# Kernel tuning notes

Hardware: AMD Instinct MI355X
Metric: run time of the kernel (lower is better)

## Reference

```python
import jax, jax.numpy as jnp
import numpy as np

N_NODES = 50000
N_EDGES = 600000
N_COMM = 500
COMM_EDGES = 8000
NFEAT = 128
NHID = 128
NCLASS = 10
NLAYERS = 3
NHEADS = 8
EPS = 1e-5


def setup_inputs() -> dict:
    key = jax.random.key(0)
    ks = jax.random.split(key, 32)
    s = 0.05
    def rn(i, shape, scale=s):
        return (jax.random.normal(ks[i], shape, dtype=jnp.float32) * scale)
    return {
        "node_features": jax.random.normal(ks[0], (N_NODES, NFEAT), dtype=jnp.float32),
        "node_edge_index": jax.random.randint(ks[1], (2, N_EDGES), 0, N_NODES),
        "comm_features": jax.random.normal(ks[2], (N_COMM, NHID), dtype=jnp.float32),
        "comm_edge_index": jax.random.randint(ks[3], (2, COMM_EDGES), 0, N_COMM),
        "node_to_comm_map": jax.random.randint(ks[4], (N_NODES,), 0, N_COMM),
        # node-branch GCN params (nfeat == nhid so weights stack)
        "node_W": rn(5, (NLAYERS, NHID, NHID)),
        "node_b": rn(6, (NLAYERS, NHID)),
        "node_bn_g": 1.0 + rn(7, (NLAYERS, NHID)),
        "node_bn_b": rn(8, (NLAYERS, NHID)),
        # community-branch GCN params
        "comm_W": rn(9, (NLAYERS, NHID, NHID)),
        "comm_b": rn(10, (NLAYERS, NHID)),
        "comm_bn_g": 1.0 + rn(11, (NLAYERS, NHID)),
        "comm_bn_b": rn(12, (NLAYERS, NHID)),
        # MultiheadAttention params (torch layout: y = x @ W.T + b)
        "attn_in_w": rn(13, (3 * NHID, NHID)),
        "attn_in_b": rn(14, (3 * NHID,)),
        "attn_out_w": rn(15, (NHID, NHID)),
        "attn_out_b": rn(16, (NHID,)),
        # gate LayerNorm
        "ln_g": 1.0 + rn(17, (NHID,)),
        "ln_b": rn(18, (NHID,)),
        # classifier: Linear(128,64) -> BN -> ReLU -> Linear(64,10)
        "cls_W1": rn(19, (NHID, NHID // 2)),
        "cls_b1": rn(20, (NHID // 2,)),
        "cls_bn_g": 1.0 + rn(21, (NHID // 2,)),
        "cls_bn_b": rn(22, (NHID // 2,)),
        "cls_W2": rn(23, (NHID // 2, NCLASS)),
        "cls_b2": rn(24, (NCLASS,)),
    }


def _gcn_norm(edge_index, n):
    # PyG gcn_norm: add self-loops, symmetric D^-1/2 (A+I) D^-1/2
    loop = jnp.arange(n)
    src = jnp.concatenate([edge_index[0], loop])
    dst = jnp.concatenate([edge_index[1], loop])
    deg = jax.ops.segment_sum(jnp.ones(src.shape[0], jnp.float32), dst, num_segments=n)
    dinv = jnp.where(deg > 0, deg ** -0.5, 0.0)
    return src, dst, dinv[src] * dinv[dst]


def _gcn_stack(x, edge_index, Ws, bs, gs, betas):
    n = x.shape[0]
    src, dst, norm = _gcn_norm(edge_index, n)
    h = x
    for i in range(Ws.shape[0]):
        h_prev = h
        m = h @ Ws[i]  # linear commutes with normalized aggregation
        agg = jax.ops.segment_sum(m[src] * norm[:, None], dst, num_segments=n) + bs[i]
        mu = agg.mean(0)
        var = agg.var(0)  # biased, as torch BN training
        hb = (agg - mu) / jnp.sqrt(var + EPS) * gs[i] + betas[i]
        h = jax.nn.relu(hb)
        if i > 0:
            h = h + h_prev
    return h


def _mha(x, wi, bi, wo, bo):
    # x: [N, S=2, E]
    N, S, E = x.shape
    dh = E // NHEADS
    qkv = x @ wi.T + bi
    q, k, v = jnp.split(qkv, 3, axis=-1)
    q = q.reshape(N, S, NHEADS, dh)
    k = k.reshape(N, S, NHEADS, dh)
    v = v.reshape(N, S, NHEADS, dh)
    att = jnp.einsum('nqhd,nkhd->nhqk', q, k) / np.float32(np.sqrt(dh))
    att = jax.nn.softmax(att, axis=-1)
    o = jnp.einsum('nhqk,nkhd->nqhd', att, v).reshape(N, S, E)
    return o @ wo.T + bo


def reference(node_features, node_edge_index, comm_features, comm_edge_index,
              node_to_comm_map, node_W, node_b, node_bn_g, node_bn_b,
              comm_W, comm_b, comm_bn_g, comm_bn_b,
              attn_in_w, attn_in_b, attn_out_w, attn_out_b,
              ln_g, ln_b, cls_W1, cls_b1, cls_bn_g, cls_bn_b, cls_W2, cls_b2):
    h_node = _gcn_stack(node_features, node_edge_index, node_W, node_b, node_bn_g, node_bn_b)
    h_comm = _gcn_stack(comm_features, comm_edge_index, comm_W, comm_b, comm_bn_g, comm_bn_b)
    safe = jnp.clip(node_to_comm_map, 0, h_comm.shape[0] - 1)
    h_comm_exp = h_comm[safe]  # [N, nhid] cross-scale gather
    comb = jnp.stack([h_node, h_comm_exp], axis=1)  # [N, 2, nhid]
    attended = _mha(comb, attn_in_w, attn_in_b, attn_out_w, attn_out_b)
    x = attended.mean(axis=1) + h_node
    mu = x.mean(-1, keepdims=True)
    var = x.var(-1, keepdims=True)
    h_final = (x - mu) / jnp.sqrt(var + EPS) * ln_g + ln_b
    z = h_final @ cls_W1 + cls_b1
    zm = z.mean(0)
    zv = z.var(0)
    z = jax.nn.relu((z - zm) / jnp.sqrt(zv + EPS) * cls_bn_g + cls_bn_b)
    logits = z @ cls_W2 + cls_b2
    return jax.nn.log_softmax(logits, axis=-1)
```

## Files before the change

kernel.cpp:

```cpp
#include <hip/hip_runtime.h>
#include <hip/hip_bf16.h>
#include <cstdint>
#include <cstddef>


typedef __attribute__((ext_vector_type(8))) short bf16x8;
typedef __attribute__((ext_vector_type(4))) float f32x4;

#define EPSV 1e-5f

__device__ __forceinline__ float b2f(unsigned short u) {
    union { unsigned int i; float f; } x; x.i = ((unsigned int)u) << 16; return x.f;
}
__device__ __forceinline__ unsigned short f2b(float f) {
    union { float f; unsigned int i; } x; x.f = f;
    unsigned int i = x.i;
    return (unsigned short)((i + 0x7fffu + ((i >> 16) & 1u)) >> 16);
}

__global__ void prep_kernel(const float* __restrict__ node_W, const float* __restrict__ comm_W,
                            const float* __restrict__ cls_W1, const float* __restrict__ attn_in_w,
                            const float* __restrict__ attn_out_w, const float* __restrict__ comm_feat,
                            const float* __restrict__ node_feat,
                            unsigned short* __restrict__ WtN, unsigned short* __restrict__ WtC,
                            unsigned short* __restrict__ W1t, unsigned short* __restrict__ WinB,
                            unsigned short* __restrict__ WoutB, unsigned short* __restrict__ cfb,
                            unsigned short* __restrict__ nfb, int nC128, int nN128) {
    int idx = blockIdx.x * 256 + threadIdx.x;
    if (idx < 49152) {
        int l = idx >> 14, e = idx & 16383;
        int j = e & 7, lane = (e >> 3) & 63, kc = (e >> 9) & 3, t = e >> 11;
        int col = t * 16 + (lane & 15);
        int k = (lane >> 4) * 8 + kc * 32 + j;
        WtN[idx] = f2b(node_W[l * 16384 + k * 128 + col]); return;
    }
    idx -= 49152;
    if (idx < 49152) {
        int l = idx >> 14, e = idx & 16383;
        int j = e & 7, lane = (e >> 3) & 63, kc = (e >> 9) & 3, t = e >> 11;
        int col = t * 16 + (lane & 15);
        int k = (lane >> 4) * 8 + kc * 32 + j;
        WtC[idx] = f2b(comm_W[l * 16384 + k * 128 + col]); return;
    }
    idx -= 49152;
    if (idx < 8192) {
        int e = idx;
        int j = e & 7, lane = (e >> 3) & 63, kc = (e >> 9) & 3, t = e >> 11;
        int col = t * 16 + (lane & 15);
        int k = (lane >> 4) * 8 + kc * 32 + j;
        W1t[idx] = f2b(cls_W1[k * 64 + col]); return;
    }
    idx -= 8192;
    if (idx < 49152) {
        int e = idx;
        int j = e & 7, lane = (e >> 3) & 63, kc = (e >> 9) & 3, t = e >> 11;
        int col = t * 16 + (lane & 15);
        int k = (lane >> 4) * 8 + kc * 32 + j;
        WinB[idx] = f2b(attn_in_w[col * 128 + k]); return;
    }
    idx -= 49152;
    if (idx < 16384) {
        int e = idx;
        int j = e & 7, lane = (e >> 3) & 63, kc = (e >> 9) & 3, t = e >> 11;
        int col = t * 16 + (lane & 15);
        int k = (lane >> 4) * 8 + kc * 32 + j;
        WoutB[idx] = f2b(attn_out_w[col * 128 + k]); return;
    }
    idx -= 16384;
    if (idx < nC128) { cfb[idx] = f2b(comm_feat[idx]); return; }
    idx -= nC128;
    if (idx < nN128) { nfb[idx] = f2b(node_feat[idx]); }
}

__global__ void count_dual(const int* __restrict__ nd, int* __restrict__ cnt_n, int nE,
                           const int* __restrict__ cd, int* __restrict__ cnt_c, int cE) {
    int t = blockIdx.x * 256 + threadIdx.x;
    if (t < nE) atomicAdd(&cnt_n[nd[t]], 1);
    else if (t - nE < cE) atomicAdd(&cnt_c[cd[t - nE]], 1);
}

__global__ void scan_block_dual(const int* __restrict__ cnt_n, int* __restrict__ rs_n,
                                int* __restrict__ bsum_n, int nN, int nbN,
                                const int* __restrict__ cnt_c, int* __restrict__ rs_c,
                                int* __restrict__ bsum_c, int nC,
                                float* __restrict__ di_n, float* __restrict__ di_c) {
    __shared__ int tmp[2048];
    int extra = (int)blockIdx.x - (nbN + (int)((nC + 1023) >> 10));
    int nbC = (nC + 1023) >> 10;
    extra = (int)blockIdx.x - (nbN + nbC);
    if (extra >= 0) {
        int g = extra * 1024 + (int)threadIdx.x;
        if (g < nN) di_n[g] = rsqrtf((float)cnt_n[g] + 1.0f);
        else { int gc = g - nN; if (gc < nC) di_c[gc] = rsqrtf((float)cnt_c[gc] + 1.0f); }
        return;
    }
    const int* cnt; int* excl; int* bsum; int n, lb;
    if ((int)blockIdx.x < nbN) { cnt = cnt_n; excl = rs_n; bsum = bsum_n; n = nN; lb = blockIdx.x; }
    else { cnt = cnt_c; excl = rs_c; bsum = bsum_c; n = nC; lb = blockIdx.x - nbN; }
    int tid = threadIdx.x;
    int gid = lb * 1024 + tid;
    int v = (gid < n) ? ((cnt[gid] + 7) & ~7) : 0;
    int buf = 0;
    tmp[tid] = v;
    __syncthreads();
    for (int d = 1; d < 1024; d <<= 1) {
        int t = tmp[buf * 1024 + tid];
        int add = (tid >= d) ? tmp[buf * 1024 + tid - d] : 0;
        tmp[(1 - buf) * 1024 + tid] = t + add;
        buf = 1 - buf;
        __syncthreads();
    }
    int inc = tmp[buf * 1024 + tid];
    if (gid < n) excl[gid] = inc - v;
    if (tid == 1023) bsum[lb] = inc;
}

__global__ void scan_sums_dual(int* __restrict__ bsum_n, int nbN,
                               int* __restrict__ bsum_c, int nbC) {
    if (threadIdx.x == 0) {
        int acc = 0;
        for (int i = 0; i < nbN; ++i) { int t = bsum_n[i]; bsum_n[i] = acc; acc += t; }
    } else if (threadIdx.x == 1) {
        int acc = 0;
        for (int i = 0; i < nbC; ++i) { int t = bsum_c[i]; bsum_c[i] = acc; acc += t; }
    }
}

__global__ void scan_add_dual(int* __restrict__ rs_n, const int* __restrict__ bsum_n,
                              int* __restrict__ cur_n, int nN,
                              int* __restrict__ rs_c, const int* __restrict__ bsum_c,
                              int* __restrict__ cur_c, int nC) {
    int gid = blockIdx.x * 256 + threadIdx.x;
    if (gid < nN) {
        int v = rs_n[gid] + bsum_n[gid >> 10];
        rs_n[gid] = v; cur_n[gid] = v;
    } else {
        int g = gid - nN;
        if (g < nC) {
            int v = rs_c[g] + bsum_c[g >> 10];
            rs_c[g] = v; cur_c[g] = v;
        }
    }
}

__global__ void fill_dual(const int* __restrict__ ns, const int* __restrict__ ndst,
                          int* __restrict__ cur_n, int* __restrict__ csrc_n, int nE,
                          const int* __restrict__ cs, const int* __restrict__ cdst,
                          int* __restrict__ cur_c, int* __restrict__ csrc_c, int cE) {
    int e = blockIdx.x * 256 + threadIdx.x;
    if (e < nE) {
        int s = ns[e], d = ndst[e];
        int pos = atomicAdd(&cur_n[d], 1);
        __builtin_nontemporal_store(s, csrc_n + pos);
    } else if (e - nE < cE) {
        int ee = e - nE;
        int s = cs[ee], d = cdst[ee];
        int pos = atomicAdd(&cur_c[d], 1);
        __builtin_nontemporal_store(s, csrc_c + pos);
    }
}

__device__ __forceinline__ void gemm_wave_128(const unsigned short* __restrict__ A,
                                              const unsigned short* __restrict__ Bt,
                                              const float* __restrict__ di,
                                              unsigned short* __restrict__ D,
                                              int M, int m0, int lane) {
    int r = lane & 15, q = lane >> 4;
    int arow = m0 + r; if (arow >= M) arow = M - 1;
    const unsigned short* ap = A + (size_t)arow * 128 + q * 8;
    bf16x8 afrag[4];
#pragma unroll
    for (int kc = 0; kc < 4; ++kc)
        afrag[kc] = *(const bf16x8*)(const void*)(ap + kc * 32);
    float dsc[4];
#pragma unroll
    for (int t = 0; t < 4; ++t) {
        int row = m0 + q * 4 + t; if (row >= M) row = M - 1;
        dsc[t] = di[row];
    }
#pragma unroll
    for (int tt = 0; tt < 8; ++tt) {
        f32x4 acc = {0.f, 0.f, 0.f, 0.f};
#pragma unroll
        for (int kc = 0; kc < 4; ++kc) {
            bf16x8 bfrag = *(const bf16x8*)(const void*)(Bt + (((size_t)tt * 4 + kc) << 9) + lane * 8);
            acc = __builtin_amdgcn_mfma_f32_16x16x32_bf16(afrag[kc], bfrag, acc, 0, 0, 0);
        }
        int n0 = tt * 16;
#pragma unroll
        for (int t = 0; t < 4; ++t) {
            int row = m0 + q * 4 + t;
            if (row < M) D[(size_t)row * 128 + n0 + r] = f2b(acc[t] * dsc[t]);
        }
    }
}

__global__ __launch_bounds__(256) void gemm_dual(
    const unsigned short* __restrict__ A0, const unsigned short* __restrict__ Bt0,
    const float* __restrict__ di0, unsigned short* __restrict__ D0, int M0, int blocksA,
    const unsigned short* __restrict__ A1, const unsigned short* __restrict__ Bt1,
    const float* __restrict__ di1, unsigned short* __restrict__ D1, int M1) {
    int blk = blockIdx.x;
    const unsigned short *A, *Bt; const float* di; unsigned short* D; int M, lb;
    if (blk < blocksA) { A = A0; Bt = Bt0; di = di0; D = D0; M = M0; lb = blk; }
    else { A = A1; Bt = Bt1; di = di1; D = D1; M = M1; lb = blk - blocksA; }
    int m0 = (lb * 4 + (int)(threadIdx.x >> 6)) * 16;
    if (m0 >= M) return;
    gemm_wave_128(A, Bt, di, D, M, m0, threadIdx.x & 63);
}

__global__ void gemm_kernel(const unsigned short* __restrict__ A,
                            const unsigned short* __restrict__ Bt,
                            const float* __restrict__ bias,
                            float* __restrict__ D, int M, int Ncol) {
    int wave = (blockIdx.x * blockDim.x + threadIdx.x) >> 6;
    int lane = threadIdx.x & 63;
    int m0 = wave * 16;
    if (m0 >= M) return;
    int r = lane & 15, q = lane >> 4;
    int arow = m0 + r; if (arow >= M) arow = M - 1;
    const unsigned short* ap = A + (size_t)arow * 128 + q * 8;
    bf16x8 afrag[4];
#pragma unroll
    for (int kc = 0; kc < 4; ++kc)
        afrag[kc] = *(const bf16x8*)(const void*)(ap + kc * 32);
    int ntiles = Ncol >> 4;
    for (int tt = 0; tt < ntiles; ++tt) {
        f32x4 acc = {0.f, 0.f, 0.f, 0.f};
#pragma unroll
        for (int kc = 0; kc < 4; ++kc) {
            bf16x8 bfrag = *(const bf16x8*)(const void*)(Bt + (((size_t)tt * 4 + kc) << 9) + lane * 8);
            acc = __builtin_amdgcn_mfma_f32_16x16x32_bf16(afrag[kc], bfrag, acc, 0, 0, 0);
        }
        int n0 = tt * 16;
        float bv = bias[n0 + r];
#pragma unroll
        for (int t = 0; t < 4; ++t) {
            int row = m0 + q * 4 + t;
            if (row < M) D[(size_t)row * Ncol + n0 + r] = acc[t] + bv;
        }
    }
}

__global__ __launch_bounds__(256) void gather_dual(
    const unsigned short* __restrict__ m0, const int* __restrict__ rs0,
    const int* __restrict__ cnt0, const int* __restrict__ cs0,
    const float* __restrict__ di0, const float* __restrict__ b0,
    float* __restrict__ agg0, float* __restrict__ bins0, int n0, int blocksA,
    const unsigned short* __restrict__ m1, const int* __restrict__ rs1,
    const int* __restrict__ cnt1, const int* __restrict__ cs1,
    const float* __restrict__ di1, const float* __restrict__ b1,
    float* __restrict__ agg1, float* __restrict__ bins1, int n1) {
    __shared__ float lsum[4][128], lsq[4][128];
    int blk = blockIdx.x;
    const unsigned short* m; const int *rs, *cnt, *cs; const float *di, *bias;
    float *agg, *bins; int n, lb;
    if (blk < blocksA) { m = m0; rs = rs0; cnt = cnt0; cs = cs0; di = di0; bias = b0; agg = agg0; bins = bins0; n = n0; lb = blk; }
    else { m = m1; rs = rs1; cnt = cnt1; cs = cs1; di = di1; bias = b1; agg = agg1; bins = bins1; n = n1; lb = blk - blocksA; }
    int wib = threadIdx.x >> 6, lane = threadIdx.x & 63;
    int node = lb * 4 + wib;
    bool act = node < n;
    float a0 = 0.f, a1 = 0.f;
    if (act) {
        int start = rs[node];
        int end = start + ((cnt[node] + 7) & ~7);
        for (int i = start; i < end; i += 8) {
            int s[8]; unsigned int v[8];
#pragma unroll
            for (int j = 0; j < 8; ++j) s[j] = cs[i + j];
#pragma unroll
            for (int j = 0; j < 8; ++j) {
                int si = s[j] < 0 ? node : s[j];
                v[j] = *(const unsigned int*)(m + (size_t)si * 128 + 2 * lane);
            }
#pragma unroll
            for (int j = 0; j < 8; ++j) {
                float wj = s[j] >= 0 ? 1.f : 0.f;
                a0 += b2f((unsigned short)(v[j] & 0xffff)) * wj;
                a1 += b2f((unsigned short)(v[j] >> 16)) * wj;
            }
        }
        unsigned int v = *(const unsigned int*)(m + (size_t)node * 128 + 2 * lane);
        a0 += b2f((unsigned short)(v & 0xffff));
        a1 += b2f((unsigned short)(v >> 16));
        float d = di[node];
        a0 = a0 * d + bias[2 * lane];
        a1 = a1 * d + bias[2 * lane + 1];
        float2 o; o.x = a0; o.y = a1;
        ((float2*)(agg + (size_t)node * 128))[lane] = o;
    }
    lsum[wib][2 * lane] = a0;       lsum[wib][2 * lane + 1] = a1;
    lsq[wib][2 * lane] = a0 * a0;   lsq[wib][2 * lane + 1] = a1 * a1;
    __syncthreads();
    int t = threadIdx.x;
    int bb = (lb & 31) * 256;
    if (t < 128) {
        float v = lsum[0][t] + lsum[1][t] + lsum[2][t] + lsum[3][t];
        atomicAdd(&bins[bb + t], v);
    } else {
        int c = t - 128;
        float v = lsq[0][c] + lsq[1][c] + lsq[2][c] + lsq[3][c];
        atomicAdd(&bins[bb + 128 + c], v);
    }
}

__global__ void stats_fin_dual(float* __restrict__ bins0, float* __restrict__ s0,
                               float* __restrict__ bins1, float* __restrict__ s1) {
    int t = threadIdx.x;
    float a = 0.f;
#pragma unroll
    for (int b = 0; b < 32; ++b) { a += bins0[b * 256 + t]; bins0[b * 256 + t] = 0.f; }
    s0[t] = a;
    float c = 0.f;
#pragma unroll
    for (int b = 0; b < 32; ++b) { c += bins1[b * 256 + t]; bins1[b * 256 + t] = 0.f; }
    s1[t] = c;
}

__global__ __launch_bounds__(256) void apply_dual(
    const float* __restrict__ agg0, const float* __restrict__ sums0,
    const float* __restrict__ g0, const float* __restrict__ be0,
    unsigned short* __restrict__ hb0, int n0, int blocksA, int useRes,
    const float* __restrict__ agg1, const float* __restrict__ sums1,
    const float* __restrict__ g1, const float* __restrict__ be1,
    unsigned short* __restrict__ hb1, int n1) {
    __shared__ float sc[128], sh[128];
    int blk = blockIdx.x;
    const float *agg, *sums, *g, *be; unsigned short* hb; int n, lb;
    if (blk < blocksA) { agg = agg0; sums = sums0; g = g0; be = be0; hb = hb0; n = n0; lb = blk; }
    else { agg = agg1; sums = sums1; g = g1; be = be1; hb = hb1; n = n1; lb = blk - blocksA; }
    int t = threadIdx.x;
    if (t < 128) {
        float inv = 1.f / (float)n;
        float mean = sums[t] * inv;
        float var = sums[128 + t] * inv - mean * mean;
        float rstd = rsqrtf(var + EPSV);
        float s = g[t] * rstd;
        sc[t] = s;
        sh[t] = be[t] - mean * s;
    }
    __syncthreads();
    int base = lb * 1024 + t * 4;
    if (base < n * 128) {
        float4 a = *(const float4*)(agg + base);
        ushort4 h = *(const ushort4*)(hb + base);
        int f = base & 127;
        float v0 = fmaxf(a.x * sc[f] + sh[f], 0.f);
        float v1 = fmaxf(a.y * sc[f + 1] + sh[f + 1], 0.f);
        float v2 = fmaxf(a.z * sc[f + 2] + sh[f + 2], 0.f);
        float v3 = fmaxf(a.w * sc[f + 3] + sh[f + 3], 0.f);
        if (useRes) { v0 += b2f(h.x); v1 += b2f(h.y); v2 += b2f(h.z); v3 += b2f(h.w); }
        ushort4 o; o.x = f2b(v0); o.y = f2b(v1); o.z = f2b(v2); o.w = f2b(v3);
        *(ushort4*)(hb + base) = o;
    }
}

__global__ __launch_bounds__(256) void mha_fused_kernel(
    const unsigned short* __restrict__ hbn, const int* __restrict__ map,
    const float* __restrict__ cqkv,
    const unsigned short* __restrict__ WinB, const float* __restrict__ bin,
    const unsigned short* __restrict__ WoutB, const float* __restrict__ bout,
    const float* __restrict__ lng, const float* __restrict__ lnb,
    unsigned short* __restrict__ hfin, int nN, int nC) {
    __shared__ unsigned short obf_s[16 * 144];
    __shared__ float att_s[16 * 132];

    int b = blockIdx.x;
    int hg = threadIdx.x >> 6;
    int lane = threadIdx.x & 63;
    int r = lane & 15, q = lane >> 4;

    int arow = b * 16 + r; if (arow >= nN) arow = nN - 1;
    const unsigned short* ap = hbn + (size_t)arow * 128 + q * 8;
    bf16x8 afrag[4];
#pragma unroll
    for (int kc = 0; kc < 4; ++kc)
        afrag[kc] = *(const bf16x8*)(const void*)(ap + kc * 32);

    const float* cp[4];
#pragma unroll
    for (int t = 0; t < 4; ++t) {
        int nt = b * 16 + q * 4 + t; if (nt >= nN) nt = nN - 1;
        int c = map[nt]; c = c < 0 ? 0 : (c >= nC ? nC - 1 : c);
        cp[t] = cqkv + (size_t)c * 384;
    }

#pragma unroll
    for (int c = 0; c < 2; ++c) {
        int h = hg * 2 + c;
        f32x4 qa, ka, va;
#pragma unroll
        for (int p = 0; p < 3; ++p) {
            int tt = p * 8 + h;
            f32x4 acc = {0.f, 0.f, 0.f, 0.f};
#pragma unroll
            for (int kc = 0; kc < 4; ++kc) {
                bf16x8 bfrag = *(const bf16x8*)(const void*)(WinB + (((size_t)tt * 4 + kc) << 9) + lane * 8);
                acc = __builtin_amdgcn_mfma_f32_16x16x32_bf16(afrag[kc], bfrag, acc, 0, 0, 0);
            }
            float bv = bin[tt * 16 + r];
#pragma unroll
            for (int t = 0; t < 4; ++t) acc[t] += bv;
            if (p == 0) qa = acc; else if (p == 1) ka = acc; else va = acc;
        }
        float qc[4], kc_[4], vc[4];
#pragma unroll
        for (int t = 0; t < 4; ++t) {
            const float* cpt = cp[t] + h * 16 + r;
            qc[t] = cpt[0]; kc_[t] = cpt[128]; vc[t] = cpt[256];
        }
#pragma unroll
        for (int t = 0; t < 4; ++t) {
            float s00 = qa[t] * ka[t];
            float s01 = qa[t] * kc_[t];
            float s10 = qc[t] * ka[t];
            float s11 = qc[t] * kc_[t];
#pragma unroll
            for (int mku = 1; mku <= 8; mku <<= 1) {
                s00 += __shfl_xor(s00, mku); s01 += __shfl_xor(s01, mku);
                s10 += __shfl_xor(s10, mku); s11 += __shfl_xor(s11, mku);
            }
            s00 *= 0.25f; s01 *= 0.25f; s10 *= 0.25f; s11 *= 0.25f;
            float m0 = fmaxf(s00, s01), m1 = fmaxf(s10, s11);
            float e00 = __expf(s00 - m0), e01 = __expf(s01 - m0);
            float e10 = __expf(s10 - m1), e11 = __expf(s11 - m1);
            float i0 = 1.f / (e00 + e01), i1 = 1.f / (e10 + e11);
            float o0 = (e00 * va[t] + e01 * vc[t]) * i0;
            float o1 = (e10 * va[t] + e11 * vc[t]) * i1;
            obf_s[(q * 4 + t) * 144 + h * 16 + r] = f2b(0.5f * (o0 + o1));
        }
    }
    __syncthreads();

    bf16x8 ofrag[4];
#pragma unroll
    for (int kc = 0; kc < 4; ++kc)
        ofrag[kc] = *(const bf16x8*)(const void*)(obf_s + r * 144 + q * 8 + kc * 32);
#pragma unroll
    for (int c = 0; c < 2; ++c) {
        int tt = hg * 2 + c;
        f32x4 acc = {0.f, 0.f, 0.f, 0.f};
#pragma unroll
        for (int kc = 0; kc < 4; ++kc) {
            bf16x8 bfrag = *(const bf16x8*)(const void*)(WoutB + (((size_t)tt * 4 + kc) << 9) + lane * 8);
            acc = __builtin_amdgcn_mfma_f32_16x16x32_bf16(ofrag[kc], bfrag, acc, 0, 0, 0);
        }
        int n0 = tt * 16;
        float bv = bout[n0 + r];
#pragma unroll
        for (int t = 0; t < 4; ++t)
            att_s[(q * 4 + t) * 132 + n0 + r] = acc[t] + bv;
    }
    __syncthreads();

    {
        int nl = threadIdx.x >> 4;
        int j = threadIdx.x & 15;
        int gnode = b * 16 + nl;
        bool ok = gnode < nN; if (!ok) gnode = nN - 1;
        const unsigned short* hrow = hbn + (size_t)gnode * 128 + j * 8;
        ushort4 ha = *(const ushort4*)(hrow);
        ushort4 hbv = *(const ushort4*)(hrow + 4);
        float x[8]; float s = 0.f, s2 = 0.f;
        x[0] = att_s[nl * 132 + j * 8 + 0] + b2f(ha.x);
        x[1] = att_s[nl * 132 + j * 8 + 1] + b2f(ha.y);
        x[2] = att_s[nl * 132 + j * 8 + 2] + b2f(ha.z);
        x[3] = att_s[nl * 132 + j * 8 + 3] + b2f(ha.w);
        x[4] = att_s[nl * 132 + j * 8 + 4] + b2f(hbv.x);
        x[5] = att_s[nl * 132 + j * 8 + 5] + b2f(hbv.y);
        x[6] = att_s[nl * 132 + j * 8 + 6] + b2f(hbv.z);
        x[7] = att_s[nl * 132 + j * 8 + 7] + b2f(hbv.w);
#pragma unroll
        for (int i = 0; i < 8; ++i) { s += x[i]; s2 += x[i] * x[i]; }
        s += __shfl_xor(s, 1);  s2 += __shfl_xor(s2, 1);
        s += __shfl_xor(s, 2);  s2 += __shfl_xor(s2, 2);
        s += __shfl_xor(s, 4);  s2 += __shfl_xor(s2, 4);
        s += __shfl_xor(s, 8);  s2 += __shfl_xor(s2, 8);
        float mu = s * (1.f / 128.f);
        float var = s2 * (1.f / 128.f) - mu * mu;
        float rstd = rsqrtf(var + EPSV);
        if (ok) {
            ushort4 o1, o2;
            o1.x = f2b((x[0] - mu) * rstd * lng[j * 8 + 0] + lnb[j * 8 + 0]);
            o1.y = f2b((x[1] - mu) * rstd * lng[j * 8 + 1] + lnb[j * 8 + 1]);
            o1.z = f2b((x[2] - mu) * rstd * lng[j * 8 + 2] + lnb[j * 8 + 2]);
            o1.w = f2b((x[3] - mu) * rstd * lng[j * 8 + 3] + lnb[j * 8 + 3]);
            o2.x = f2b((x[4] - mu) * rstd * lng[j * 8 + 4] + lnb[j * 8 + 4]);
            o2.y = f2b((x[5] - mu) * rstd * lng[j * 8 + 5] + lnb[j * 8 + 5]);
            o2.z = f2b((x[6] - mu) * rstd * lng[j * 8 + 6] + lnb[j * 8 + 6]);
            o2.w = f2b((x[7] - mu) * rstd * lng[j * 8 + 7] + lnb[j * 8 + 7]);
            *(ushort4*)(hfin + (size_t)gnode * 128 + j * 8) = o1;
            *(ushort4*)(hfin + (size_t)gnode * 128 + j * 8 + 4) = o2;
        }
    }
}

__global__ __launch_bounds__(256) void stats64_kernel(const float* __restrict__ z,
                                                      float* __restrict__ sums, int N) {
    __shared__ float ls[4][64], lsq[4][64];
    int f = threadIdx.x & 63, rg = threadIdx.x >> 6;
    int r0 = blockIdx.x * 64 + rg * 16;
    int r1 = r0 + 16; if (r1 > N) r1 = N;
    float s = 0.f, s2 = 0.f;
    for (int r = r0; r < r1; ++r) {
        float v = z[(size_t)r * 64 + f];
        s += v; s2 += v * v;
    }
    ls[rg][f] = s; lsq[rg][f] = s2;
    __syncthreads();
    int t = threadIdx.x;
    if (t < 64) atomicAdd(&sums[t], ls[0][t] + ls[1][t] + ls[2][t] + ls[3][t]);
    else if (t < 128) { int c = t - 64; atomicAdd(&sums[64 + c], lsq[0][c] + lsq[1][c] + lsq[2][c] + lsq[3][c]); }
}

__global__ __launch_bounds__(256) void final_kernel(const float* __restrict__ z,
                                                    const float* __restrict__ sums,
                                                    const float* __restrict__ g,
                                                    const float* __restrict__ be,
                                                    const float* __restrict__ W2,
                                                    const float* __restrict__ b2v,
                                                    float* __restrict__ out, int nN) {
    int node = blockIdx.x * 4 + (threadIdx.x >> 6);
    int lane = threadIdx.x & 63;
    float inv = 1.f / (float)nN;
    float mean = sums[lane] * inv;
    float var = sums[64 + lane] * inv - mean * mean;
    float sc = g[lane] * rsqrtf(var + EPSV);
    float sh = be[lane] - mean * sc;
    float v = 0.f;
    if (node < nN) v = fmaxf(z[(size_t)node * 64 + lane] * sc + sh, 0.f);
    float p[10];
    const float* wrow = W2 + lane * 10;
#pragma unroll
    for (int c = 0; c < 10; ++c) p[c] = v * wrow[c];
#pragma unroll
    for (int off = 32; off >= 1; off >>= 1) {
#pragma unroll
        for (int c = 0; c < 10; ++c) p[c] += __shfl_xor(p[c], off);
    }
    if (node >= nN) return;
    float l[10], mx = -1e30f;
#pragma unroll
    for (int c = 0; c < 10; ++c) { l[c] = p[c] + b2v[c]; mx = fmaxf(mx, l[c]); }
    float se = 0.f;
#pragma unroll
    for (int c = 0; c < 10; ++c) se += expf(l[c] - mx);
    float lse = mx + logf(se);
    if (lane < 10) out[(size_t)node * 10 + lane] = l[lane] - lse;
}

static inline int cdiv(long a, long b) { return (int)((a + b - 1) / b); }

extern "C" void kernel_launch(void* const* d_in, const int* in_sizes, int n_in,
                              void* d_out, int out_size, void* d_ws, size_t ws_size,
                              hipStream_t stream) {
    const float* node_feat = (const float*)d_in[0];
    const int*   nedge     = (const int*)d_in[1];
    const float* comm_feat = (const float*)d_in[2];
    const int*   cedge     = (const int*)d_in[3];
    const int*   n2c       = (const int*)d_in[4];
    const float* node_W    = (const float*)d_in[5];
    const float* node_b    = (const float*)d_in[6];
    const float* node_g    = (const float*)d_in[7];
    const float* node_beta = (const float*)d_in[8];
    const float* comm_W    = (const float*)d_in[9];
    const float* comm_b    = (const float*)d_in[10];
    const float* comm_g    = (const float*)d_in[11];
    const float* comm_beta = (const float*)d_in[12];
    const float* attn_in_w = (const float*)d_in[13];
    const float* attn_in_b = (const float*)d_in[14];
    const float* attn_out_w= (const float*)d_in[15];
    const float* attn_out_b= (const float*)d_in[16];
    const float* ln_g      = (const float*)d_in[17];
    const float* ln_b      = (const float*)d_in[18];
    const float* cls_W1    = (const float*)d_in[19];
    const float* cls_b1    = (const float*)d_in[20];
    const float* cls_bn_g  = (const float*)d_in[21];
    const float* cls_bn_b  = (const float*)d_in[22];
    const float* cls_W2    = (const float*)d_in[23];
    const float* cls_b2    = (const float*)d_in[24];

    const int nN = in_sizes[0] / 128;
    const int nE = in_sizes[1] / 2;
    const int nC = in_sizes[2] / 128;
    const int cE = in_sizes[3] / 2;
    const int padE_n = nE + 8 * nN;
    const int padE_c = cE + 8 * nC;

    char* ws = (char*)d_ws;
    size_t off = 0;
    auto alloc = [&](size_t bytes) -> char* {
        char* p = ws + off;
        off = (off + bytes + 255) & ~(size_t)255;
        return p;
    };
    size_t zero_begin = off;
    int*   cnt_n  = (int*)alloc((size_t)nN * 4);
    int*   cur_n  = (int*)alloc((size_t)nN * 4);
    int*   cnt_c  = (int*)alloc((size_t)nC * 4);
    int*   cur_c  = (int*)alloc((size_t)nC * 4);
    float* gsums  = (float*)alloc((size_t)6 * 256 * 4);
    float* csums  = (float*)alloc(128 * 4);
    float* bins_n = (float*)alloc((size_t)32 * 256 * 4);
    float* bins_c = (float*)alloc((size_t)32 * 256 * 4);
    size_t zero_bytes = off - zero_begin;
    size_t neg_begin = off;
    int*   csrc_n = (int*)alloc((size_t)padE_n * 4);
    int*   csrc_c = (int*)alloc((size_t)padE_c * 4);
    size_t neg_bytes = off - neg_begin;
    int*   rs_n   = (int*)alloc((size_t)(nN + 1) * 4);
    int*   bsum_n = (int*)alloc(256 * 4);
    float* dinv_n = (float*)alloc((size_t)nN * 4);
    int*   rs_c   = (int*)alloc((size_t)(nC + 1) * 4);
    int*   bsum_c = (int*)alloc(256 * 4);
    float* dinv_c = (float*)alloc((size_t)nC * 4);
    unsigned short* hb_n  = (unsigned short*)alloc((size_t)nN * 256);
    unsigned short* hb_c  = (unsigned short*)alloc((size_t)nC * 256);
    unsigned short* cfb   = (unsigned short*)alloc((size_t)nC * 256);
    unsigned short* m_cb  = (unsigned short*)alloc((size_t)nC * 256);
    float*          agg_c = (float*)alloc((size_t)nC * 512);
    float*          cqkv  = (float*)alloc((size_t)nC * 384 * 4);
    unsigned short* WtN  = (unsigned short*)alloc((size_t)3 * 16384 * 2);
    unsigned short* WtC  = (unsigned short*)alloc((size_t)3 * 16384 * 2);
    unsigned short* W1t  = (unsigned short*)alloc((size_t)64 * 128 * 2);
    unsigned short* WinB = (unsigned short*)alloc((size_t)384 * 128 * 2);
    unsigned short* WoutB= (unsigned short*)alloc((size_t)128 * 128 * 2);
    unsigned short* m_nb = (unsigned short*)alloc((size_t)nN * 256);
    float*          agg_n= (float*)alloc((size_t)nN * 512);
    unsigned short* nfb  = (unsigned short*)agg_n;
    unsigned short* hfin = m_nb;
    float*          z    = agg_n;

    hipMemsetAsync(ws + zero_begin, 0, zero_bytes, stream);
    hipMemsetAsync(ws + neg_begin, 0xFF, neg_bytes, stream);

    long prepN = 49152L * 3 + 8192 + 16384 + (long)nC * 128 + (long)nN * 128;
    prep_kernel<<<cdiv(prepN, 256), 256, 0, stream>>>(
        node_W, comm_W, cls_W1, attn_in_w, attn_out_w, comm_feat, node_feat,
        WtN, WtC, W1t, WinB, WoutB, cfb, nfb, nC * 128, nN * 128);

    count_dual<<<cdiv((long)nE + cE, 256), 256, 0, stream>>>(nedge + nE, cnt_n, nE, cedge + cE, cnt_c, cE);
    int nbN = cdiv(nN, 1024), nbC = cdiv(nC, 1024);
    int dinvB = cdiv((long)nN + nC, 1024);
    scan_block_dual<<<nbN + nbC + dinvB, 1024, 0, stream>>>(
        cnt_n, rs_n, bsum_n, nN, nbN, cnt_c, rs_c, bsum_c, nC, dinv_n, dinv_c);
    scan_sums_dual<<<1, 64, 0, stream>>>(bsum_n, nbN, bsum_c, nbC);
    scan_add_dual<<<cdiv((long)nN + nC, 256), 256, 0, stream>>>(
        rs_n, bsum_n, cur_n, nN, rs_c, bsum_c, cur_c, nC);
    fill_dual<<<cdiv((long)nE + cE, 256), 256, 0, stream>>>(
        nedge, nedge + nE, cur_n, csrc_n, nE,
        cedge, cedge + cE, cur_c, csrc_c, cE);

    int gemmA = cdiv(nN, 64), gemmB = cdiv(nC, 64);
    int gatA = cdiv(nN, 4), gatB = cdiv(nC, 4);
    int appA = cdiv((long)nN * 128, 1024), appB = cdiv((long)nC * 128, 1024);
    for (int i = 0; i < 3; ++i) {
        const unsigned short* A0 = i == 0 ? nfb : hb_n;
        const unsigned short* A1 = i == 0 ? cfb : hb_c;
        float* s0 = gsums + (size_t)(i * 2 + 0) * 256;
        float* s1 = gsums + (size_t)(i * 2 + 1) * 256;
        gemm_dual<<<gemmA + gemmB, 256, 0, stream>>>(
            A0, WtN + i * 16384, dinv_n, m_nb, nN, gemmA,
            A1, WtC + i * 16384, dinv_c, m_cb, nC);
        gather_dual<<<gatA + gatB, 256, 0, stream>>>(
            m_nb, rs_n, cnt_n, csrc_n, dinv_n, node_b + i * 128, agg_n, bins_n, nN, gatA,
            m_cb, rs_c, cnt_c, csrc_c, dinv_c, comm_b + i * 128, agg_c, bins_c, nC);
        stats_fin_dual<<<1, 256, 0, stream>>>(bins_n, s0, bins_c, s1);
        apply_dual<<<appA + appB, 256, 0, stream>>>(
            agg_n, s0, node_g + i * 128, node_beta + i * 128, hb_n, nN, appA, i > 0 ? 1 : 0,
            agg_c, s1, comm_g + i * 128, comm_beta + i * 128, hb_c, nC);
    }

    int cwaves = cdiv(nC, 16);
    gemm_kernel<<<cdiv((long)cwaves * 64, 256), 256, 0, stream>>>(
        hb_c, WinB, attn_in_b, cqkv, nC, 384);

    mha_fused_kernel<<<cdiv(nN, 16), 256, 0, stream>>>(
        hb_n, n2c, cqkv, WinB, attn_in_b, WoutB, attn_out_b, ln_g, ln_b, hfin, nN, nC);

    int waves1 = (nN + 15) / 16;
    gemm_kernel<<<cdiv((long)waves1 * 64, 256), 256, 0, stream>>>(
        hfin, W1t, cls_b1, z, nN, 64);
    stats64_kernel<<<cdiv(nN, 64), 256, 0, stream>>>(z, csums, nN);
    final_kernel<<<cdiv(nN, 4), 256, 0, stream>>>(z, csums, cls_bn_g, cls_bn_b,
                                                  cls_W2, cls_b2, (float*)d_out, nN);
}
```

Measured before the change: 508.3 us.

## Give each wave its own 16-node tile in fused MHA and drop block barriers

The fused attention kernel now assigns one 16-node tile per wave, with four tiles per block, instead of splitting 8 heads across 4 waves of a single tile. Each wave computes all heads, its own output projection and the LayerNorm in registers using shuffles. This removes the two block-wide syncs and the float staging buffer in shared memory. In exchange each wave does four times more MFMA work per tile and reloads all weight fragments. The residual reads and output writes become scalar 2-byte accesses rather than vectorized ones.

```diff
diff --git a/kernel.cpp b/kernel.cpp
--- a/kernel.cpp
+++ b/kernel.cpp
@@ -85,9 +85,8 @@
                                 int* __restrict__ bsum_c, int nC,
                                 float* __restrict__ di_n, float* __restrict__ di_c) {
     __shared__ int tmp[2048];
-    int extra = (int)blockIdx.x - (nbN + (int)((nC + 1023) >> 10));
     int nbC = (nC + 1023) >> 10;
-    extra = (int)blockIdx.x - (nbN + nbC);
+    int extra = (int)blockIdx.x - (nbN + nbC);
     if (extra >= 0) {
         int g = extra * 1024 + (int)threadIdx.x;
         if (g < nN) di_n[g] = rsqrtf((float)cnt_n[g] + 1.0f);
@@ -362,15 +361,14 @@
     const unsigned short* __restrict__ WoutB, const float* __restrict__ bout,
     const float* __restrict__ lng, const float* __restrict__ lnb,
     unsigned short* __restrict__ hfin, int nN, int nC) {
-    __shared__ unsigned short obf_s[16 * 144];
-    __shared__ float att_s[16 * 132];
-
-    int b = blockIdx.x;
-    int hg = threadIdx.x >> 6;
+    __shared__ unsigned short obf_s[4][16 * 136];
+
+    int w = threadIdx.x >> 6;
     int lane = threadIdx.x & 63;
     int r = lane & 15, q = lane >> 4;
-
-    int arow = b * 16 + r; if (arow >= nN) arow = nN - 1;
+    int gbase = blockIdx.x * 64 + w * 16;
+
+    int arow = gbase + r; if (arow >= nN) arow = nN - 1;
     const unsigned short* ap = hbn + (size_t)arow * 128 + q * 8;
     bf16x8 afrag[4];
 #pragma unroll
@@ -380,14 +378,15 @@
     const float* cp[4];
 #pragma unroll
     for (int t = 0; t < 4; ++t) {
-        int nt = b * 16 + q * 4 + t; if (nt >= nN) nt = nN - 1;
+        int nt = gbase + q * 4 + t; if (nt >= nN) nt = nN - 1;
         int c = map[nt]; c = c < 0 ? 0 : (c >= nC ? nC - 1 : c);
         cp[t] = cqkv + (size_t)c * 384;
     }
 
-#pragma unroll
-    for (int c = 0; c < 2; ++c) {
-        int h = hg * 2 + c;
+    unsigned short* obf = obf_s[w];
+
+#pragma unroll 2
+    for (int h = 0; h < 8; ++h) {
         f32x4 qa, ka, va;
 #pragma unroll
         for (int p = 0; p < 3; ++p) {
@@ -427,70 +426,55 @@
             float i0 = 1.f / (e00 + e01), i1 = 1.f / (e10 + e11);
             float o0 = (e00 * va[t] + e01 * vc[t]) * i0;
             float o1 = (e10 * va[t] + e11 * vc[t]) * i1;
-            obf_s[(q * 4 + t) * 144 + h * 16 + r] = f2b(0.5f * (o0 + o1));
-        }
-    }
-    __syncthreads();
+            obf[(q * 4 + t) * 136 + h * 16 + r] = f2b(0.5f * (o0 + o1));
+        }
+    }
 
     bf16x8 ofrag[4];
 #pragma unroll
     for (int kc = 0; kc < 4; ++kc)
-        ofrag[kc] = *(const bf16x8*)(const void*)(obf_s + r * 144 + q * 8 + kc * 32);
-#pragma unroll
-    for (int c = 0; c < 2; ++c) {
-        int tt = hg * 2 + c;
+        ofrag[kc] = *(const bf16x8*)(const void*)(obf + r * 136 + q * 8 + kc * 32);
+    float x[8][4];
+    float sm[4] = {0.f, 0.f, 0.f, 0.f}, sq[4] = {0.f, 0.f, 0.f, 0.f};
+#pragma unroll
+    for (int tt = 0; tt < 8; ++tt) {
         f32x4 acc = {0.f, 0.f, 0.f, 0.f};
 #pragma unroll
         for (int kc = 0; kc < 4; ++kc) {
             bf16x8 bfrag = *(const bf16x8*)(const void*)(WoutB + (((size_t)tt * 4 + kc) << 9) + lane * 8);
             acc = __builtin_amdgcn_mfma_f32_16x16x32_bf16(ofrag[kc], bfrag, acc, 0, 0, 0);
         }
-        int n0 = tt * 16;
-        float bv = bout[n0 + r];
-#pragma unroll
-        for (int t = 0; t < 4; ++t)
-            att_s[(q * 4 + t) * 132 + n0 + r] = acc[t] + bv;
-    }
-    __syncthreads();
-
-    {
-        int nl = threadIdx.x >> 4;
-        int j = threadIdx.x & 15;
-        int gnode = b * 16 + nl;
-        bool ok = gnode < nN; if (!ok) gnode = nN - 1;
-        const unsigned short* hrow = hbn + (size_t)gnode * 128 + j * 8;
-        ushort4 ha = *(const ushort4*)(hrow);
-        ushort4 hbv = *(const ushort4*)(hrow + 4);
-        float x[8]; float s = 0.f, s2 = 0.f;
-        x[0] = att_s[nl * 132 + j * 8 + 0] + b2f(ha.x);
-        x[1] = att_s[nl * 132 + j * 8 + 1] + b2f(ha.y);
-        x[2] = att_s[nl * 132 + j * 8 + 2] + b2f(ha.z);
-        x[3] = att_s[nl * 132 + j * 8 + 3] + b2f(ha.w);
-        x[4] = att_s[nl * 132 + j * 8 + 4] + b2f(hbv.x);
-        x[5] = att_s[nl * 132 + j * 8 + 5] + b2f(hbv.y);
-        x[6] = att_s[nl * 132 + j * 8 + 6] + b2f(hbv.z);
-        x[7] = att_s[nl * 132 + j * 8 + 7] + b2f(hbv.w);
-#pragma unroll
-        for (int i = 0; i < 8; ++i) { s += x[i]; s2 += x[i] * x[i]; }
-        s += __shfl_xor(s, 1);  s2 += __shfl_xor(s2, 1);
-        s += __shfl_xor(s, 2);  s2 += __shfl_xor(s2, 2);
-        s += __shfl_xor(s, 4);  s2 += __shfl_xor(s2, 4);
-        s += __shfl_xor(s, 8);  s2 += __shfl_xor(s2, 8);
-        float mu = s * (1.f / 128.f);
-        float var = s2 * (1.f / 128.f) - mu * mu;
-        float rstd = rsqrtf(var + EPSV);
-        if (ok) {
-            ushort4 o1, o2;
-            o1.x = f2b((x[0] - mu) * rstd * lng[j * 8 + 0] + lnb[j * 8 + 0]);
-            o1.y = f2b((x[1] - mu) * rstd * lng[j * 8 + 1] + lnb[j * 8 + 1]);
-            o1.z = f2b((x[2] - mu) * rstd * lng[j * 8 + 2] + lnb[j * 8 + 2]);
-            o1.w = f2b((x[3] - mu) * rstd * lng[j * 8 + 3] + lnb[j * 8 + 3]);
-            o2.x = f2b((x[4] - mu) * rstd * lng[j * 8 + 4] + lnb[j * 8 + 4]);
-            o2.y = f2b((x[5] - mu) * rstd * lng[j * 8 + 5] + lnb[j * 8 + 5]);
-            o2.z = f2b((x[6] - mu) * rstd * lng[j * 8 + 6] + lnb[j * 8 + 6]);
-            o2.w = f2b((x[7] - mu) * rstd * lng[j * 8 + 7] + lnb[j * 8 + 7]);
-            *(ushort4*)(hfin + (size_t)gnode * 128 + j * 8) = o1;
-            *(ushort4*)(hfin + (size_t)gnode * 128 + j * 8 + 4) = o2;
+        float bv = bout[tt * 16 + r];
+#pragma unroll
+        for (int t = 0; t < 4; ++t) {
+            int row = gbase + q * 4 + t; if (row >= nN) row = nN - 1;
+            float xv = acc[t] + bv + b2f(hbn[(size_t)row * 128 + tt * 16 + r]);
+            x[tt][t] = xv; sm[t] += xv; sq[t] += xv * xv;
+        }
+    }
+#pragma unroll
+    for (int mku = 1; mku <= 8; mku <<= 1) {
+#pragma unroll
+        for (int t = 0; t < 4; ++t) {
+            sm[t] += __shfl_xor(sm[t], mku);
+            sq[t] += __shfl_xor(sq[t], mku);
+        }
+    }
+    float mu[4], rsd[4];
+#pragma unroll
+    for (int t = 0; t < 4; ++t) {
+        mu[t] = sm[t] * (1.f / 128.f);
+        float var = sq[t] * (1.f / 128.f) - mu[t] * mu[t];
+        rsd[t] = rsqrtf(var + EPSV);
+    }
+#pragma unroll
+    for (int tt = 0; tt < 8; ++tt) {
+        float lg = lng[tt * 16 + r], lb = lnb[tt * 16 + r];
+#pragma unroll
+        for (int t = 0; t < 4; ++t) {
+            int row = gbase + q * 4 + t;
+            if (row < nN)
+                hfin[(size_t)row * 128 + tt * 16 + r] = f2b((x[tt][t] - mu[t]) * rsd[t] * lg + lb);
         }
     }
 }
@@ -675,7 +659,7 @@
     gemm_kernel<<<cdiv((long)cwaves * 64, 256), 256, 0, stream>>>(
         hb_c, WinB, attn_in_b, cqkv, nC, 384);
 
-    mha_fused_kernel<<<cdiv(nN, 16), 256, 0, stream>>>(
+    mha_fused_kernel<<<cdiv(nN, 64), 256, 0, stream>>>(
         hb_n, n2c, cqkv, WinB, attn_in_b, WoutB, attn_out_b, ln_g, ln_b, hfin, nN, nC);
 
     int waves1 = (nN + 15) / 16;
```

New measurement: 521.9 us. 1.03x slower.

## Fuse classifier Linear1 and BN statistics into the MHA kernel epilogue

Applied to the files above, without the earlier changes.

The LayerNorm output now stays in shared memory inside the MHA kernel, where an MFMA multiplies it by W1 and writes z directly. Per-column sums and squared sums are gathered into 32 binned atomic buffers and folded by a small finalize kernel. This drops the write and re-read of hfin, the separate GEMM launch, and the stats64 kernel that re-read z. In exchange the MHA kernel does more work and needs an extra barrier, and the atomic binning changes the order of the floating-point reduction.

```diff
diff --git a/kernel.cpp b/kernel.cpp
--- a/kernel.cpp
+++ b/kernel.cpp
@@ -85,9 +85,8 @@
                                 int* __restrict__ bsum_c, int nC,
                                 float* __restrict__ di_n, float* __restrict__ di_c) {
     __shared__ int tmp[2048];
-    int extra = (int)blockIdx.x - (nbN + (int)((nC + 1023) >> 10));
     int nbC = (nC + 1023) >> 10;
-    extra = (int)blockIdx.x - (nbN + nbC);
+    int extra = (int)blockIdx.x - (nbN + nbC);
     if (extra >= 0) {
         int g = extra * 1024 + (int)threadIdx.x;
         if (g < nN) di_n[g] = rsqrtf((float)cnt_n[g] + 1.0f);
@@ -361,7 +360,8 @@
     const unsigned short* __restrict__ WinB, const float* __restrict__ bin,
     const unsigned short* __restrict__ WoutB, const float* __restrict__ bout,
     const float* __restrict__ lng, const float* __restrict__ lnb,
-    unsigned short* __restrict__ hfin, int nN, int nC) {
+    const unsigned short* __restrict__ W1t, const float* __restrict__ b1v,
+    float* __restrict__ z, float* __restrict__ zbins, int nN, int nC) {
     __shared__ unsigned short obf_s[16 * 144];
     __shared__ float att_s[16 * 132];
 
@@ -452,12 +452,13 @@
             att_s[(q * 4 + t) * 132 + n0 + r] = acc[t] + bv;
     }
     __syncthreads();
+    unsigned short* hf_s = obf_s;
 
     {
         int nl = threadIdx.x >> 4;
         int j = threadIdx.x & 15;
         int gnode = b * 16 + nl;
-        bool ok = gnode < nN; if (!ok) gnode = nN - 1;
+        if (gnode >= nN) gnode = nN - 1;
         const unsigned short* hrow = hbn + (size_t)gnode * 128 + j * 8;
         ushort4 ha = *(const ushort4*)(hrow);
         ushort4 hbv = *(const ushort4*)(hrow + 4);
@@ -479,38 +480,58 @@
         float mu = s * (1.f / 128.f);
         float var = s2 * (1.f / 128.f) - mu * mu;
         float rstd = rsqrtf(var + EPSV);
-        if (ok) {
-            ushort4 o1, o2;
-            o1.x = f2b((x[0] - mu) * rstd * lng[j * 8 + 0] + lnb[j * 8 + 0]);
-            o1.y = f2b((x[1] - mu) * rstd * lng[j * 8 + 1] + lnb[j * 8 + 1]);
-            o1.z = f2b((x[2] - mu) * rstd * lng[j * 8 + 2] + lnb[j * 8 + 2]);
-            o1.w = f2b((x[3] - mu) * rstd * lng[j * 8 + 3] + lnb[j * 8 + 3]);
-            o2.x = f2b((x[4] - mu) * rstd * lng[j * 8 + 4] + lnb[j * 8 + 4]);
-            o2.y = f2b((x[5] - mu) * rstd * lng[j * 8 + 5] + lnb[j * 8 + 5]);
-            o2.z = f2b((x[6] - mu) * rstd * lng[j * 8 + 6] + lnb[j * 8 + 6]);
-            o2.w = f2b((x[7] - mu) * rstd * lng[j * 8 + 7] + lnb[j * 8 + 7]);
-            *(ushort4*)(hfin + (size_t)gnode * 128 + j * 8) = o1;
-            *(ushort4*)(hfin + (size_t)gnode * 128 + j * 8 + 4) = o2;
-        }
-    }
-}
-
-__global__ __launch_bounds__(256) void stats64_kernel(const float* __restrict__ z,
-                                                      float* __restrict__ sums, int N) {
-    __shared__ float ls[4][64], lsq[4][64];
-    int f = threadIdx.x & 63, rg = threadIdx.x >> 6;
-    int r0 = blockIdx.x * 64 + rg * 16;
-    int r1 = r0 + 16; if (r1 > N) r1 = N;
-    float s = 0.f, s2 = 0.f;
-    for (int r = r0; r < r1; ++r) {
-        float v = z[(size_t)r * 64 + f];
-        s += v; s2 += v * v;
-    }
-    ls[rg][f] = s; lsq[rg][f] = s2;
+        ushort4 o1, o2;
+        o1.x = f2b((x[0] - mu) * rstd * lng[j * 8 + 0] + lnb[j * 8 + 0]);
+        o1.y = f2b((x[1] - mu) * rstd * lng[j * 8 + 1] + lnb[j * 8 + 1]);
+        o1.z = f2b((x[2] - mu) * rstd * lng[j * 8 + 2] + lnb[j * 8 + 2]);
+        o1.w = f2b((x[3] - mu) * rstd * lng[j * 8 + 3] + lnb[j * 8 + 3]);
+        o2.x = f2b((x[4] - mu) * rstd * lng[j * 8 + 4] + lnb[j * 8 + 4]);
+        o2.y = f2b((x[5] - mu) * rstd * lng[j * 8 + 5] + lnb[j * 8 + 5]);
+        o2.z = f2b((x[6] - mu) * rstd * lng[j * 8 + 6] + lnb[j * 8 + 6]);
+        o2.w = f2b((x[7] - mu) * rstd * lng[j * 8 + 7] + lnb[j * 8 + 7]);
+        *(ushort4*)(hf_s + nl * 136 + j * 8) = o1;
+        *(ushort4*)(hf_s + nl * 136 + j * 8 + 4) = o2;
+    }
     __syncthreads();
+
+    {
+        bf16x8 hfrag[4];
+#pragma unroll
+        for (int kc = 0; kc < 4; ++kc)
+            hfrag[kc] = *(const bf16x8*)(const void*)(hf_s + r * 136 + q * 8 + kc * 32);
+        f32x4 acc = {0.f, 0.f, 0.f, 0.f};
+#pragma unroll
+        for (int kc = 0; kc < 4; ++kc) {
+            bf16x8 bfrag = *(const bf16x8*)(const void*)(W1t + (((size_t)hg * 4 + kc) << 9) + lane * 8);
+            acc = __builtin_amdgcn_mfma_f32_16x16x32_bf16(hfrag[kc], bfrag, acc, 0, 0, 0);
+        }
+        float bv = b1v[hg * 16 + r];
+        float s = 0.f, s2 = 0.f;
+#pragma unroll
+        for (int t = 0; t < 4; ++t) {
+            int row = b * 16 + q * 4 + t;
+            if (row < nN) {
+                float v = acc[t] + bv;
+                z[(size_t)row * 64 + hg * 16 + r] = v;
+                s += v; s2 += v * v;
+            }
+        }
+        s += __shfl_xor(s, 16);  s2 += __shfl_xor(s2, 16);
+        s += __shfl_xor(s, 32);  s2 += __shfl_xor(s2, 32);
+        if (lane < 16) {
+            int bb = (b & 31) * 128;
+            atomicAdd(&zbins[bb + hg * 16 + r], s);
+            atomicAdd(&zbins[bb + 64 + hg * 16 + r], s2);
+        }
+    }
+}
+
+__global__ void stats_fin_z(const float* __restrict__ bins, float* __restrict__ s) {
     int t = threadIdx.x;
-    if (t < 64) atomicAdd(&sums[t], ls[0][t] + ls[1][t] + ls[2][t] + ls[3][t]);
-    else if (t < 128) { int c = t - 64; atomicAdd(&sums[64 + c], lsq[0][c] + lsq[1][c] + lsq[2][c] + lsq[3][c]); }
+    float a = 0.f;
+#pragma unroll
+    for (int b = 0; b < 32; ++b) a += bins[b * 128 + t];
+    s[t] = a;
 }
 
 __global__ __launch_bounds__(256) void final_kernel(const float* __restrict__ z,
@@ -603,6 +624,7 @@
     float* csums  = (float*)alloc(128 * 4);
     float* bins_n = (float*)alloc((size_t)32 * 256 * 4);
     float* bins_c = (float*)alloc((size_t)32 * 256 * 4);
+    float* zbins  = (float*)alloc((size_t)32 * 128 * 4);
     size_t zero_bytes = off - zero_begin;
     size_t neg_begin = off;
     int*   csrc_n = (int*)alloc((size_t)padE_n * 4);
@@ -628,7 +650,6 @@
     unsigned short* m_nb = (unsigned short*)alloc((size_t)nN * 256);
     float*          agg_n= (float*)alloc((size_t)nN * 512);
     unsigned short* nfb  = (unsigned short*)agg_n;
-    unsigned short* hfin = m_nb;
     float*          z    = agg_n;
 
     hipMemsetAsync(ws + zero_begin, 0, zero_bytes, stream);
@@ -676,12 +697,10 @@
         hb_c, WinB, attn_in_b, cqkv, nC, 384);
 
     mha_fused_kernel<<<cdiv(nN, 16), 256, 0, stream>>>(
-        hb_n, n2c, cqkv, WinB, attn_in_b, WoutB, attn_out_b, ln_g, ln_b, hfin, nN, nC);
-
-    int waves1 = (nN + 15) / 16;
-    gemm_kernel<<<cdiv((long)waves1 * 64, 256), 256, 0, stream>>>(
-        hfin, W1t, cls_b1, z, nN, 64);
-    stats64_kernel<<<cdiv(nN, 64), 256, 0, stream>>>(z, csums, nN);
+        hb_n, n2c, cqkv, WinB, attn_in_b, WoutB, attn_out_b, ln_g, ln_b,
+        W1t, cls_b1, z, zbins, nN, nC);
+
+    stats_fin_z<<<1, 128, 0, stream>>>(zbins, csums);
     final_kernel<<<cdiv(nN, 4), 256, 0, stream>>>(z, csums, cls_bn_g, cls_bn_b,
                                                   cls_W2, cls_b2, (float*)d_out, nN);
 }
```

Measured after the change: 483.2 us. 1.05x faster.
